# Kernel optimization log

Hardware: AMD Instinct MI355X
Metric: run time of the kernel (lower is better)

## Reference

```python
import jax, jax.numpy as jnp
import numpy as np

T, N, E = 8, 10000, 200000
F_IN, H, OUT = 32, 128, 64
EPS = 1e-5


def setup_inputs() -> dict:
    key = jax.random.key(0)
    ks = jax.random.split(key, 28)
    inp = {}
    inp['x'] = jax.random.normal(ks[0], (T, N, F_IN), jnp.float32)
    inp['edge_index'] = jax.random.randint(ks[1], (2, E), 0, N, dtype=jnp.int32)
    # GCN layer weights (Glorot-ish scale)
    inp['w_gcn0'] = jax.random.normal(ks[2], (F_IN, H), jnp.float32) / np.float32(np.sqrt(F_IN))
    inp['b_gcn0'] = jnp.zeros((H,), jnp.float32)
    inp['w_gcn1'] = jax.random.normal(ks[3], (H, H), jnp.float32) / np.float32(np.sqrt(H))
    inp['b_gcn1'] = jnp.zeros((H,), jnp.float32)
    inp['w_gcn2'] = jax.random.normal(ks[4], (H, H), jnp.float32) / np.float32(np.sqrt(H))
    inp['b_gcn2'] = jnp.zeros((H,), jnp.float32)
    # BatchNorm (eval mode) params for the two inner norms
    for i, kb in zip(range(2), range(5, 9, 2)):
        inp[f'bn_g{i}'] = 1.0 + 0.1 * jax.random.normal(ks[kb], (H,), jnp.float32)
        inp[f'bn_b{i}'] = 0.1 * jax.random.normal(ks[kb + 1], (H,), jnp.float32)
        inp[f'bn_m{i}'] = 0.1 * jax.random.normal(ks[kb + 10], (H,), jnp.float32)
        inp[f'bn_v{i}'] = jax.random.uniform(ks[kb + 11], (H,), jnp.float32, 0.5, 1.5)
    # 3-layer LSTM params, torch gate order (i, f, g, o)
    s = np.float32(1.0 / np.sqrt(OUT))
    dims_in = [H, OUT, OUT]
    for l in range(3):
        k0, k1, k2, k3 = jax.random.split(ks[20 + l], 4)
        inp[f'w_ih_{l}'] = jax.random.uniform(k0, (4 * OUT, dims_in[l]), jnp.float32, -s, s)
        inp[f'w_hh_{l}'] = jax.random.uniform(k1, (4 * OUT, OUT), jnp.float32, -s, s)
        inp[f'b_ih_{l}'] = jax.random.uniform(k2, (4 * OUT,), jnp.float32, -s, s)
        inp[f'b_hh_{l}'] = jax.random.uniform(k3, (4 * OUT,), jnp.float32, -s, s)
    return inp


def reference(x, edge_index, w_gcn0, b_gcn0, w_gcn1, b_gcn1, w_gcn2, b_gcn2,
              bn_g0, bn_b0, bn_m0, bn_v0, bn_g1, bn_b1, bn_m1, bn_v1,
              w_ih_0, w_hh_0, b_ih_0, b_hh_0,
              w_ih_1, w_hh_1, b_ih_1, b_hh_1,
              w_ih_2, w_hh_2, b_ih_2, b_hh_2):
    src, dst = edge_index[0], edge_index[1]
    # symmetric GCN normalization with self-loops: deg = in-degree + 1
    deg = jax.ops.segment_sum(jnp.ones((E,), x.dtype), dst, num_segments=N) + 1.0
    dis = jax.lax.rsqrt(deg)
    coef = dis[src] * dis[dst]          # [E] edge norm
    self_w = dis * dis                   # [N] self-loop norm

    def gcn(h, W, b):
        hw = jnp.einsum('tnf,fo->tno', h, W)                      # [T,N,O]
        msg = hw[:, src, :] * coef[None, :, None]                  # [T,E,O]
        agg = jax.vmap(lambda m: jax.ops.segment_sum(m, dst, num_segments=N))(msg)
        return agg + hw * self_w[None, :, None] + b

    def bn(h, g, b_, m, v):  # eval-mode BatchNorm1d
        return (h - m) * (g * jax.lax.rsqrt(v + EPS)) + b_

    h = bn(jax.nn.relu(gcn(x, w_gcn0, b_gcn0)), bn_g0, bn_b0, bn_m0, bn_v0)
    h = bn(jax.nn.relu(gcn(h, w_gcn1, b_gcn1)), bn_g1, bn_b1, bn_m1, bn_v1)
    h = jax.nn.relu(gcn(h, w_gcn2, b_gcn2))                        # [T,N,H]

    def lstm_layer(xs, Wih, Whh, bih, bhh):
        Hd = Whh.shape[1]
        bias = bih + bhh
        def step(carry, xt):
            hp, cp = carry
            g = xt @ Wih.T + hp @ Whh.T + bias
            i, f, gg, o = jnp.split(g, 4, axis=-1)
            c = jax.nn.sigmoid(f) * cp + jax.nn.sigmoid(i) * jnp.tanh(gg)
            hn = jax.nn.sigmoid(o) * jnp.tanh(c)
            return (hn, c), hn
        z = jnp.zeros((xs.shape[1], Hd), xs.dtype)
        _, ys = jax.lax.scan(step, (z, z), xs)
        return ys  # [T,N,Hd]

    ys = lstm_layer(h, w_ih_0, w_hh_0, b_ih_0, b_hh_0)
    ys = lstm_layer(ys, w_ih_1, w_hh_1, b_ih_1, b_hh_1)
    ys = lstm_layer(ys, w_ih_2, w_hh_2, b_ih_2, b_hh_2)
    return ys[-1]  # [N, OUT] == x[:, -1, :] in the torch code
```

## Files before the change

kernel.cpp:

```cpp
#include <hip/hip_runtime.h>
#include <hip/hip_bf16.h>
#include <math.h>

#define NTHREADS 256
#define T_STEPS 8
#define F_INC 32
#define H_DIM 128
#define O_DIM 64

typedef unsigned short u16;
typedef __attribute__((ext_vector_type(8))) short short8_t;
typedef __attribute__((ext_vector_type(4))) float float4_t;

__device__ __forceinline__ float bf2f(u16 u) {
    return __uint_as_float(((unsigned)u) << 16);
}
__device__ __forceinline__ u16 f2bf(float f) {
    __hip_bfloat16 h = __float2bfloat16(f);
    union { __hip_bfloat16 h; u16 s; } cv; cv.h = h; return cv.s;
}
__device__ __forceinline__ float4 ld_bf4(const u16* p) {
    uint2 u = *(const uint2*)p;
    return make_float4(__uint_as_float(u.x << 16), __uint_as_float(u.x & 0xffff0000u),
                       __uint_as_float(u.y << 16), __uint_as_float(u.y & 0xffff0000u));
}
__device__ __forceinline__ void st_bf4(u16* p, float4 v) {
    ushort4 s = make_ushort4(f2bf(v.x), f2bf(v.y), f2bf(v.z), f2bf(v.w));
    *(ushort4*)p = s;
}
__device__ __forceinline__ float fsig(float x) {
    float xc = fminf(fmaxf(x, -30.f), 30.f);
    float e = __builtin_amdgcn_exp2f(xc * -1.4426950408889634f);
    return __builtin_amdgcn_rcpf(1.0f + e);
}
__device__ __forceinline__ float ftanh(float x) {
    float xc = fminf(fmaxf(x, -15.f), 15.f);
    float e = __builtin_amdgcn_exp2f(xc * -2.8853900817779268f);
    float r = __builtin_amdgcn_rcpf(1.0f + e);
    return fmaf(-2.0f * e, r, 1.0f);
}

__global__ void init_cnt_kernel(int* __restrict__ cnt, int n) {
    int i = blockIdx.x * NTHREADS + threadIdx.x;
    if (i < n) cnt[i] = 0;
}

__global__ void count_kernel(const int* __restrict__ ei, int* __restrict__ cnt, int E) {
    int e = blockIdx.x * NTHREADS + threadIdx.x;
    if (e < E) atomicAdd(&cnt[ei[E + e]], 1);
}

__global__ void scan_part1(const int* __restrict__ cnt, int* __restrict__ bsum, int n) {
    __shared__ int sd[NTHREADS];
    const int i = blockIdx.x * NTHREADS + threadIdx.x;
    sd[threadIdx.x] = (i < n) ? cnt[i] : 0;
    __syncthreads();
    for (int off = 128; off > 0; off >>= 1) {
        if (threadIdx.x < off) sd[threadIdx.x] += sd[threadIdx.x + off];
        __syncthreads();
    }
    if (threadIdx.x == 0) bsum[blockIdx.x] = sd[0];
}
__global__ void scan_part2(const int* __restrict__ bsum, int* __restrict__ boff, int nb) {
    if (threadIdx.x == 0) {
        int s = 0;
        for (int b = 0; b < nb; ++b) { boff[b] = s; s += bsum[b]; }
    }
}
__global__ void scan_part3(const int* __restrict__ cnt, const int* __restrict__ boff,
                           int* __restrict__ rowptr, int* __restrict__ wp,
                           float* __restrict__ dis, float* __restrict__ selfw, int n) {
    __shared__ int sd[NTHREADS];
    const int i = blockIdx.x * NTHREADS + threadIdx.x;
    const int v = (i < n) ? cnt[i] : 0;
    sd[threadIdx.x] = v;
    __syncthreads();
    for (int off = 1; off < NTHREADS; off <<= 1) {
        const int tv = (threadIdx.x >= off) ? sd[threadIdx.x - off] : 0;
        __syncthreads();
        sd[threadIdx.x] += tv;
        __syncthreads();
    }
    const int excl = boff[blockIdx.x] + sd[threadIdx.x] - v;
    if (i < n) {
        rowptr[i] = excl; wp[i] = excl;
        if (i == n - 1) rowptr[n] = excl + v;
        const float d = 1.0f + (float)v;
        dis[i] = rsqrtf(d);
        selfw[i] = 1.0f / d;
    }
}

__global__ void fill_kernel(const int* __restrict__ ei, const float* __restrict__ dis,
                            int* __restrict__ wp, int* __restrict__ csr_src,
                            float* __restrict__ coefA, int E) {
    int e = blockIdx.x * NTHREADS + threadIdx.x;
    if (e < E) {
        int s = ei[e], d = ei[E + e];
        int p = atomicAdd(&wp[d], 1);
        csr_src[p] = s;
        coefA[p] = dis[s] * dis[d];
    }
}

__global__ void wprep_all_kernel(const float* g0, const float* g1, const float* g2,
                                 const float* i0, const float* i1, const float* i2,
                                 const float* h0, const float* h1, const float* h2,
                                 u16* o_g0, u16* o_g1, u16* o_g2,
                                 u16* o_i0, u16* o_i1, u16* o_i2,
                                 u16* o_h0, u16* o_h1, u16* o_h2) {
    const int i = blockIdx.x * NTHREADS + threadIdx.x;
    if (i < 4096)        { o_g0[i] = f2bf(g0[(i & 31) * 128 + (i >> 5)]); }
    else if (i < 20480)  { int j = i - 4096;   o_g1[j] = f2bf(g1[(j & 127) * 128 + (j >> 7)]); }
    else if (i < 36864)  { int j = i - 20480;  o_g2[j] = f2bf(g2[(j & 127) * 128 + (j >> 7)]); }
    else if (i < 69632)  { int j = i - 36864;  o_i0[j] = f2bf(i0[j]); }
    else if (i < 86016)  { int j = i - 69632;  o_i1[j] = f2bf(i1[j]); }
    else if (i < 102400) { int j = i - 86016;  o_i2[j] = f2bf(i2[j]); }
    else if (i < 118784) { int j = i - 102400; o_h0[j] = f2bf(h0[j]); }
    else if (i < 135168) { int j = i - 118784; o_h1[j] = f2bf(h1[j]); }
    else if (i < 151552) { int j = i - 135168; o_h2[j] = f2bf(h2[j]); }
}

__global__ __launch_bounds__(NTHREADS)
void agg32t_kernel(const float* __restrict__ x, const int* __restrict__ rowptr,
                   const int* __restrict__ csrc, const float* __restrict__ coefA,
                   const float* __restrict__ selfw, u16* __restrict__ out, int N) {
    const int t = blockIdx.x;
    const int slot = threadIdx.x >> 3, lane = threadIdx.x & 7;
    const int n = blockIdx.y * 32 + slot;
    if (n >= N) return;
    const int c4 = lane * 4;
    const float* xb = x + (long)t * N * 32;
    const int e0 = rowptr[n], e1 = rowptr[n + 1];
    const float sw = selfw[n];
    const float4 sv = *(const float4*)(xb + (long)n * 32 + c4);
    float4 acc = make_float4(sw * sv.x, sw * sv.y, sw * sv.z, sw * sv.w);
    for (int e = e0; e < e1; ++e) {
        const float wgt = coefA[e];
        const int s = csrc[e];
        const float4 v = *(const float4*)(xb + (long)s * 32 + c4);
        acc.x = fmaf(wgt, v.x, acc.x);
        acc.y = fmaf(wgt, v.y, acc.y);
        acc.z = fmaf(wgt, v.z, acc.z);
        acc.w = fmaf(wgt, v.w, acc.w);
    }
    st_bf4(out + ((long)t * N + n) * 32 + c4, acc);
}

__global__ __launch_bounds__(NTHREADS)
void agg128t_kernel(const u16* __restrict__ h, const int* __restrict__ rowptr,
                    const int* __restrict__ csrc, const float* __restrict__ coefA,
                    const float* __restrict__ selfw, u16* __restrict__ out, int N) {
    const int t = blockIdx.x;
    const int slot = threadIdx.x >> 5, lane = threadIdx.x & 31;
    const int n = blockIdx.y * 8 + slot;
    const int c4 = lane * 4;
    const u16* hb = h + (long)t * N * 128;
    const int e0 = rowptr[n], e1 = rowptr[n + 1];
    const float sw = selfw[n];
    const float4 sv = ld_bf4(hb + (long)n * 128 + c4);
    float4 acc = make_float4(sw * sv.x, sw * sv.y, sw * sv.z, sw * sv.w);
    for (int e = e0; e < e1; ++e) {
        const float wgt = coefA[e];
        const int s = csrc[e];
        const float4 v = ld_bf4(hb + (long)s * 128 + c4);
        acc.x = fmaf(wgt, v.x, acc.x);
        acc.y = fmaf(wgt, v.y, acc.y);
        acc.z = fmaf(wgt, v.z, acc.z);
        acc.w = fmaf(wgt, v.w, acc.w);
    }
    st_bf4(out + ((long)t * N + n) * 128 + c4, acc);
}

template<int K, int EPI, bool OUTBF>
__global__ __launch_bounds__(NTHREADS)
void mfma_gemm_kernel(const u16* __restrict__ A, const u16* __restrict__ Bt,
                      const float* __restrict__ bias0,
                      const float* __restrict__ bng, const float* __restrict__ bnb,
                      const float* __restrict__ bnm, const float* __restrict__ bnv,
                      void* __restrict__ Cout, int ldc) {
    constexpr int KC = (K < 64) ? K : 64;
    constexpr int KP = KC + 8;
    constexpr int KV = KC / 8;
    __shared__ __align__(16) u16 As[128 * KP];
    __shared__ __align__(16) u16 Bs[128 * KP];
    const int tid = threadIdx.x;
    const long row0 = (long)blockIdx.x * 128;
    const int col0 = blockIdx.y * 128;
    const int wid = tid >> 6, lane = tid & 63;
    const int quad = lane >> 4, l16 = lane & 15;

    float4_t acc[2][8];
    #pragma unroll
    for (int rt = 0; rt < 2; ++rt)
        #pragma unroll
        for (int ct = 0; ct < 8; ++ct)
            acc[rt][ct] = (float4_t){0.f, 0.f, 0.f, 0.f};

    const int arow = wid * 32 + l16;
    const int koff = quad * 8;
    for (int ch = 0; ch < K / KC; ++ch) {
        const int kbase = ch * KC;
        for (int p = tid; p < 128 * KV; p += NTHREADS) {
            const int r = p / KV, kv = p % KV;
            *(uint4*)(&As[r * KP + kv * 8]) =
                *(const uint4*)(A + (row0 + r) * K + kbase + kv * 8);
        }
        for (int p = tid; p < 128 * KV; p += NTHREADS) {
            const int r = p / KV, kv = p % KV;
            *(uint4*)(&Bs[r * KP + kv * 8]) =
                *(const uint4*)(Bt + (long)(col0 + r) * K + kbase + kv * 8);
        }
        __syncthreads();
        #pragma unroll
        for (int kc = 0; kc < KC / 32; ++kc) {
            const short8_t a0 = *(const short8_t*)(&As[arow * KP + kc * 32 + koff]);
            const short8_t a1 = *(const short8_t*)(&As[(arow + 16) * KP + kc * 32 + koff]);
            #pragma unroll
            for (int ct = 0; ct < 8; ++ct) {
                const short8_t b = *(const short8_t*)(&Bs[(ct * 16 + l16) * KP + kc * 32 + koff]);
                acc[0][ct] = __builtin_amdgcn_mfma_f32_16x16x32_bf16(a0, b, acc[0][ct], 0, 0, 0);
                acc[1][ct] = __builtin_amdgcn_mfma_f32_16x16x32_bf16(a1, b, acc[1][ct], 0, 0, 0);
            }
        }
        __syncthreads();
    }

    float e_add0[8], e_mul[8], e_add1[8];
    #pragma unroll
    for (int ct = 0; ct < 8; ++ct) {
        const int c = col0 + ct * 16 + l16;
        e_add0[ct] = bias0[c];
        if constexpr (EPI == 2) {
            const float s = bng[c] * rsqrtf(bnv[c] + 1e-5f);
            e_mul[ct] = s;
            e_add1[ct] = bnb[c] - bnm[c] * s;
        }
    }
    #pragma unroll
    for (int rt = 0; rt < 2; ++rt) {
        #pragma unroll
        for (int r = 0; r < 4; ++r) {
            const long row = row0 + wid * 32 + rt * 16 + quad * 4 + r;
            #pragma unroll
            for (int ct = 0; ct < 8; ++ct) {
                float v = fmaxf(acc[rt][ct][r] + e_add0[ct], 0.f);
                if constexpr (EPI == 2) v = fmaf(v, e_mul[ct], e_add1[ct]);
                const long idx = row * (long)ldc + col0 + ct * 16 + l16;
                if constexpr (OUTBF) ((u16*)Cout)[idx] = f2bf(v);
                else ((float*)Cout)[idx] = v;
            }
        }
    }
}

template<int KIN, bool IN_SPLIT, bool LAST>
__global__ __launch_bounds__(NTHREADS, 2)
void lstm_layer_kernel(const u16* __restrict__ in_hi, const u16* __restrict__ in_lo,
                       const u16* __restrict__ wih, const u16* __restrict__ whh,
                       const float* __restrict__ bi, const float* __restrict__ bh,
                       u16* __restrict__ out_hi, u16* __restrict__ out_lo,
                       float* __restrict__ out_f, int N) {
    constexpr int NKS = KIN / 32;
    constexpr int HSTR = 76;
    const int tid = threadIdx.x;
    const int w = tid >> 6, lane = tid & 63;
    const int quad = lane >> 4, l16 = lane & 15;
    const int n0 = blockIdx.x * 16;
    const int u = w * 16 + l16;

    __shared__ __align__(16) u16 hT[2][16][HSTR];
    for (int p = tid; p < 2 * 16 * HSTR; p += NTHREADS) (&hT[0][0][0])[p] = 0;

    short8_t fI[4][NKS], fH[4][2];
    #pragma unroll
    for (int g = 0; g < 4; ++g) {
        #pragma unroll
        for (int ks = 0; ks < NKS; ++ks)
            fI[g][ks] = *(const short8_t*)(wih + (long)(g * 64 + u) * KIN + ks * 32 + quad * 8);
        #pragma unroll
        for (int ks = 0; ks < 2; ++ks)
            fH[g][ks] = *(const short8_t*)(whh + (long)(g * 64 + u) * 64 + ks * 32 + quad * 8);
    }
    float bias[4];
    #pragma unroll
    for (int g = 0; g < 4; ++g) bias[g] = bi[g * 64 + u] + bh[g * 64 + u];
    float cst[4] = {};
    __syncthreads();

    #pragma unroll 1
    for (int t = 0; t < T_STEPS; ++t) {
        short8_t ain[NKS], ainl[NKS];
        const long ibase = ((long)t * N + n0 + l16) * KIN + quad * 8;
        #pragma unroll
        for (int ks = 0; ks < NKS; ++ks) {
            ain[ks] = *(const short8_t*)(in_hi + ibase + ks * 32);
            if constexpr (IN_SPLIT) ainl[ks] = *(const short8_t*)(in_lo + ibase + ks * 32);
        }
        short8_t ah[2], al[2];
        #pragma unroll
        for (int ks = 0; ks < 2; ++ks) {
            ah[ks] = *(const short8_t*)(&hT[0][l16][ks * 32 + quad * 8]);
            al[ks] = *(const short8_t*)(&hT[1][l16][ks * 32 + quad * 8]);
        }
        __syncthreads();

        float4_t acc[4];
        #pragma unroll
        for (int g = 0; g < 4; ++g) acc[g] = (float4_t){bias[g], bias[g], bias[g], bias[g]};
        #pragma unroll
        for (int ks = 0; ks < NKS; ++ks)
            #pragma unroll
            for (int g = 0; g < 4; ++g) {
                acc[g] = __builtin_amdgcn_mfma_f32_16x16x32_bf16(ain[ks], fI[g][ks], acc[g], 0, 0, 0);
                if constexpr (IN_SPLIT)
                    acc[g] = __builtin_amdgcn_mfma_f32_16x16x32_bf16(ainl[ks], fI[g][ks], acc[g], 0, 0, 0);
            }
        #pragma unroll
        for (int ks = 0; ks < 2; ++ks)
            #pragma unroll
            for (int g = 0; g < 4; ++g) {
                acc[g] = __builtin_amdgcn_mfma_f32_16x16x32_bf16(ah[ks], fH[g][ks], acc[g], 0, 0, 0);
                acc[g] = __builtin_amdgcn_mfma_f32_16x16x32_bf16(al[ks], fH[g][ks], acc[g], 0, 0, 0);
            }

        #pragma unroll
        for (int r = 0; r < 4; ++r) {
            const float si = fsig(acc[0][r]);
            const float sf = fsig(acc[1][r]);
            const float gg = ftanh(acc[2][r]);
            const float so = fsig(acc[3][r]);
            const float c = sf * cst[r] + si * gg;
            cst[r] = c;
            const float h = so * ftanh(c);
            const int node = quad * 4 + r;
            const u16 hi = f2bf(h);
            const u16 lo = f2bf(h - bf2f(hi));
            hT[0][node][u] = hi;
            hT[1][node][u] = lo;
            if constexpr (LAST) {
                if (t == T_STEPS - 1) out_f[(long)(n0 + node) * 64 + u] = h;
            } else {
                const long o = ((long)t * N + n0 + node) * 64 + u;
                out_hi[o] = hi;
                out_lo[o] = lo;
            }
        }
        __syncthreads();
    }
}

extern "C" void kernel_launch(void* const* d_in, const int* in_sizes, int n_in,
                              void* d_out, int out_size, void* d_ws, size_t ws_size,
                              hipStream_t stream) {
    (void)n_in; (void)out_size; (void)ws_size;
    const float* x      = (const float*)d_in[0];
    const int*   ei     = (const int*)d_in[1];
    const float* w_gcn0 = (const float*)d_in[2];
    const float* b_gcn0 = (const float*)d_in[3];
    const float* w_gcn1 = (const float*)d_in[4];
    const float* b_gcn1 = (const float*)d_in[5];
    const float* w_gcn2 = (const float*)d_in[6];
    const float* b_gcn2 = (const float*)d_in[7];
    const float* bn_g0  = (const float*)d_in[8];
    const float* bn_b0  = (const float*)d_in[9];
    const float* bn_m0  = (const float*)d_in[10];
    const float* bn_v0  = (const float*)d_in[11];
    const float* bn_g1  = (const float*)d_in[12];
    const float* bn_b1  = (const float*)d_in[13];
    const float* bn_m1  = (const float*)d_in[14];
    const float* bn_v1  = (const float*)d_in[15];
    const float* w_ih_0 = (const float*)d_in[16];
    const float* w_hh_0 = (const float*)d_in[17];
    const float* b_ih_0 = (const float*)d_in[18];
    const float* b_hh_0 = (const float*)d_in[19];
    const float* w_ih_1 = (const float*)d_in[20];
    const float* w_hh_1 = (const float*)d_in[21];
    const float* b_ih_1 = (const float*)d_in[22];
    const float* b_hh_1 = (const float*)d_in[23];
    const float* w_ih_2 = (const float*)d_in[24];
    const float* w_hh_2 = (const float*)d_in[25];
    const float* b_ih_2 = (const float*)d_in[26];
    const float* b_hh_2 = (const float*)d_in[27];

    const int E = in_sizes[1] / 2;
    const int N = in_sizes[0] / (T_STEPS * F_INC);
    const long M = (long)N * T_STEPS;

    char* ws = (char*)d_ws;
    size_t off = 0;
    auto carve = [&](size_t bytes) -> void* {
        void* p = ws + off;
        off += (bytes + 255) & ~(size_t)255;
        return p;
    };
    float* dis     = (float*)carve((size_t)N * 4);
    float* selfw   = (float*)carve((size_t)N * 4);
    float* coefA   = (float*)carve((size_t)E * 4);
    int*   cnt     = (int*)carve((size_t)N * 4);
    int*   rowptr  = (int*)carve((size_t)(N + 1) * 4);
    int*   wp      = (int*)carve((size_t)N * 4);
    int*   csr_src = (int*)carve((size_t)E * 4);
    int*   bsum    = (int*)carve(64 * 4);
    int*   boff    = (int*)carve(64 * 4);
    u16*   hbuf    = (u16*)carve((size_t)M * H_DIM * 2);
    u16*   abuf    = (u16*)carve((size_t)M * H_DIM * 2);
    u16*   pA_hi   = (u16*)carve((size_t)M * O_DIM * 2);
    u16*   pA_lo   = (u16*)carve((size_t)M * O_DIM * 2);
    u16*   pB_hi   = (u16*)carve((size_t)M * O_DIM * 2);
    u16*   pB_lo   = (u16*)carve((size_t)M * O_DIM * 2);
    u16*   wt0     = (u16*)carve((size_t)128 * 32 * 2);
    u16*   wt1     = (u16*)carve((size_t)128 * 128 * 2);
    u16*   wt2     = (u16*)carve((size_t)128 * 128 * 2);
    u16*   wtih0   = (u16*)carve((size_t)256 * 128 * 2);
    u16*   wtih1   = (u16*)carve((size_t)256 * 64 * 2);
    u16*   wtih2   = (u16*)carve((size_t)256 * 64 * 2);
    u16*   whh0b   = (u16*)carve((size_t)256 * 64 * 2);
    u16*   whh1b   = (u16*)carve((size_t)256 * 64 * 2);
    u16*   whh2b   = (u16*)carve((size_t)256 * 64 * 2);

    const dim3 b256(NTHREADS);
    const int gN = (N + NTHREADS - 1) / NTHREADS;
    const int gE = (E + NTHREADS - 1) / NTHREADS;

    init_cnt_kernel<<<gN, b256, 0, stream>>>(cnt, N);
    count_kernel<<<gE, b256, 0, stream>>>(ei, cnt, E);
    scan_part1<<<gN, b256, 0, stream>>>(cnt, bsum, N);
    scan_part2<<<1, 64, 0, stream>>>(bsum, boff, gN);
    scan_part3<<<gN, b256, 0, stream>>>(cnt, boff, rowptr, wp, dis, selfw, N);
    fill_kernel<<<gE, b256, 0, stream>>>(ei, dis, wp, csr_src, coefA, E);

    wprep_all_kernel<<<(151552 + 255) / 256, b256, 0, stream>>>(
        w_gcn0, w_gcn1, w_gcn2, w_ih_0, w_ih_1, w_ih_2, w_hh_0, w_hh_1, w_hh_2,
        wt0, wt1, wt2, wtih0, wtih1, wtih2, whh0b, whh1b, whh2b);

    const int gBlk = (int)(M / 128);
    agg32t_kernel<<<dim3(T_STEPS, (N + 31) / 32), b256, 0, stream>>>(
        x, rowptr, csr_src, coefA, selfw, abuf, N);
    mfma_gemm_kernel<32, 2, true><<<dim3(gBlk, 1), b256, 0, stream>>>(
        abuf, wt0, b_gcn0, bn_g0, bn_b0, bn_m0, bn_v0, hbuf, 128);
    agg128t_kernel<<<dim3(T_STEPS, N / 8), b256, 0, stream>>>(
        hbuf, rowptr, csr_src, coefA, selfw, abuf, N);
    mfma_gemm_kernel<128, 2, true><<<dim3(gBlk, 1), b256, 0, stream>>>(
        abuf, wt1, b_gcn1, bn_g1, bn_b1, bn_m1, bn_v1, hbuf, 128);
    agg128t_kernel<<<dim3(T_STEPS, N / 8), b256, 0, stream>>>(
        hbuf, rowptr, csr_src, coefA, selfw, abuf, N);
    mfma_gemm_kernel<128, 1, true><<<dim3(gBlk, 1), b256, 0, stream>>>(
        abuf, wt2, b_gcn2, nullptr, nullptr, nullptr, nullptr, hbuf, 128);

    const int gL = N / 16;
    lstm_layer_kernel<128, false, false><<<gL, b256, 0, stream>>>(
        hbuf, nullptr, wtih0, whh0b, b_ih_0, b_hh_0, pA_hi, pA_lo, nullptr, N);
    lstm_layer_kernel<64, true, false><<<gL, b256, 0, stream>>>(
        pA_hi, pA_lo, wtih1, whh1b, b_ih_1, b_hh_1, pB_hi, pB_lo, nullptr, N);
    lstm_layer_kernel<64, true, true><<<gL, b256, 0, stream>>>(
        pB_hi, pB_lo, wtih2, whh2b, b_ih_2, b_hh_2, nullptr, nullptr, (float*)d_out, N);
}
```

Before: 426.5 us.

## Split neighbor edges across lanes in GCN aggregation with shuffle reduction

Both aggregation kernels now assign one wavefront per node and spread that node's incoming edges over several lane groups (8 groups for the 32-wide features, 4 for the 128-wide), then combine the partial sums with xor shuffles. The 128-wide kernel also switches to 16-byte loads of 8 bf16 values per lane. The aim is more gathers in flight per node, since each node averages about 20 edges, which shortens the serial per-edge dependency chain and raises memory-level parallelism. The cost is shuffle reduction overhead and idle lanes for low-degree nodes. The grid size assumes N is divisible by 4.

Result: faster. 377.6 us (-11.5%).

```diff
diff --git a/kernel.cpp b/kernel.cpp
--- a/kernel.cpp
+++ b/kernel.cpp
@@ -27,6 +27,12 @@
 __device__ __forceinline__ void st_bf4(u16* p, float4 v) {
     ushort4 s = make_ushort4(f2bf(v.x), f2bf(v.y), f2bf(v.z), f2bf(v.w));
     *(ushort4*)p = s;
+}
+__device__ __forceinline__ void bf8_unpack(uint4 u, float* f) {
+    f[0] = __uint_as_float(u.x << 16); f[1] = __uint_as_float(u.x & 0xffff0000u);
+    f[2] = __uint_as_float(u.y << 16); f[3] = __uint_as_float(u.y & 0xffff0000u);
+    f[4] = __uint_as_float(u.z << 16); f[5] = __uint_as_float(u.z & 0xffff0000u);
+    f[6] = __uint_as_float(u.w << 16); f[7] = __uint_as_float(u.w & 0xffff0000u);
 }
 __device__ __forceinline__ float fsig(float x) {
     float xc = fminf(fmaxf(x, -30.f), 30.f);
@@ -126,25 +132,36 @@
                    const int* __restrict__ csrc, const float* __restrict__ coefA,
                    const float* __restrict__ selfw, u16* __restrict__ out, int N) {
     const int t = blockIdx.x;
-    const int slot = threadIdx.x >> 3, lane = threadIdx.x & 7;
-    const int n = blockIdx.y * 32 + slot;
-    if (n >= N) return;
-    const int c4 = lane * 4;
+    const int n = blockIdx.y * 4 + (threadIdx.x >> 6);
+    const int lane = threadIdx.x & 63;
+    const int split = lane >> 3;
+    const int c4 = (lane & 7) * 4;
     const float* xb = x + (long)t * N * 32;
     const int e0 = rowptr[n], e1 = rowptr[n + 1];
-    const float sw = selfw[n];
-    const float4 sv = *(const float4*)(xb + (long)n * 32 + c4);
-    float4 acc = make_float4(sw * sv.x, sw * sv.y, sw * sv.z, sw * sv.w);
-    for (int e = e0; e < e1; ++e) {
+    float a[4] = {};
+    #pragma unroll 2
+    for (int e = e0 + split; e < e1; e += 8) {
         const float wgt = coefA[e];
         const int s = csrc[e];
         const float4 v = *(const float4*)(xb + (long)s * 32 + c4);
-        acc.x = fmaf(wgt, v.x, acc.x);
-        acc.y = fmaf(wgt, v.y, acc.y);
-        acc.z = fmaf(wgt, v.z, acc.z);
-        acc.w = fmaf(wgt, v.w, acc.w);
-    }
-    st_bf4(out + ((long)t * N + n) * 32 + c4, acc);
+        a[0] = fmaf(wgt, v.x, a[0]);
+        a[1] = fmaf(wgt, v.y, a[1]);
+        a[2] = fmaf(wgt, v.z, a[2]);
+        a[3] = fmaf(wgt, v.w, a[3]);
+    }
+    #pragma unroll
+    for (int j = 0; j < 4; ++j) {
+        a[j] += __shfl_xor(a[j], 8);
+        a[j] += __shfl_xor(a[j], 16);
+        a[j] += __shfl_xor(a[j], 32);
+    }
+    if (split == 0) {
+        const float sw = selfw[n];
+        const float4 sv = *(const float4*)(xb + (long)n * 32 + c4);
+        float4 r = make_float4(fmaf(sw, sv.x, a[0]), fmaf(sw, sv.y, a[1]),
+                               fmaf(sw, sv.z, a[2]), fmaf(sw, sv.w, a[3]));
+        st_bf4(out + ((long)t * N + n) * 32 + c4, r);
+    }
 }
 
 __global__ __launch_bounds__(NTHREADS)
@@ -152,24 +169,42 @@
                     const int* __restrict__ csrc, const float* __restrict__ coefA,
                     const float* __restrict__ selfw, u16* __restrict__ out, int N) {
     const int t = blockIdx.x;
-    const int slot = threadIdx.x >> 5, lane = threadIdx.x & 31;
-    const int n = blockIdx.y * 8 + slot;
-    const int c4 = lane * 4;
+    const int n = blockIdx.y * 4 + (threadIdx.x >> 6);
+    const int lane = threadIdx.x & 63;
+    const int split = lane >> 4;
+    const int c8 = (lane & 15) * 8;
     const u16* hb = h + (long)t * N * 128;
     const int e0 = rowptr[n], e1 = rowptr[n + 1];
-    const float sw = selfw[n];
-    const float4 sv = ld_bf4(hb + (long)n * 128 + c4);
-    float4 acc = make_float4(sw * sv.x, sw * sv.y, sw * sv.z, sw * sv.w);
-    for (int e = e0; e < e1; ++e) {
+    float a[8] = {};
+    #pragma unroll 2
+    for (int e = e0 + split; e < e1; e += 4) {
         const float wgt = coefA[e];
         const int s = csrc[e];
-        const float4 v = ld_bf4(hb + (long)s * 128 + c4);
-        acc.x = fmaf(wgt, v.x, acc.x);
-        acc.y = fmaf(wgt, v.y, acc.y);
-        acc.z = fmaf(wgt, v.z, acc.z);
-        acc.w = fmaf(wgt, v.w, acc.w);
-    }
-    st_bf4(out + ((long)t * N + n) * 128 + c4, acc);
+        const uint4 v = *(const uint4*)(hb + (long)s * 128 + c8);
+        float f[8];
+        bf8_unpack(v, f);
+        #pragma unroll
+        for (int j = 0; j < 8; ++j) a[j] = fmaf(wgt, f[j], a[j]);
+    }
+    #pragma unroll
+    for (int j = 0; j < 8; ++j) {
+        a[j] += __shfl_xor(a[j], 16);
+        a[j] += __shfl_xor(a[j], 32);
+    }
+    if (split == 0) {
+        const float sw = selfw[n];
+        const uint4 sv = *(const uint4*)(hb + (long)n * 128 + c8);
+        float f[8];
+        bf8_unpack(sv, f);
+        ushort4 o0, o1;
+        o0.x = f2bf(fmaf(sw, f[0], a[0])); o0.y = f2bf(fmaf(sw, f[1], a[1]));
+        o0.z = f2bf(fmaf(sw, f[2], a[2])); o0.w = f2bf(fmaf(sw, f[3], a[3]));
+        o1.x = f2bf(fmaf(sw, f[4], a[4])); o1.y = f2bf(fmaf(sw, f[5], a[5]));
+        o1.z = f2bf(fmaf(sw, f[6], a[6])); o1.w = f2bf(fmaf(sw, f[7], a[7]));
+        u16* op = out + ((long)t * N + n) * 128 + c8;
+        *(ushort4*)op = o0;
+        *(ushort4*)(op + 4) = o1;
+    }
 }
 
 template<int K, int EPI, bool OUTBF>
@@ -435,15 +470,15 @@
         wt0, wt1, wt2, wtih0, wtih1, wtih2, whh0b, whh1b, whh2b);
 
     const int gBlk = (int)(M / 128);
-    agg32t_kernel<<<dim3(T_STEPS, (N + 31) / 32), b256, 0, stream>>>(
+    agg32t_kernel<<<dim3(T_STEPS, N / 4), b256, 0, stream>>>(
         x, rowptr, csr_src, coefA, selfw, abuf, N);
     mfma_gemm_kernel<32, 2, true><<<dim3(gBlk, 1), b256, 0, stream>>>(
         abuf, wt0, b_gcn0, bn_g0, bn_b0, bn_m0, bn_v0, hbuf, 128);
-    agg128t_kernel<<<dim3(T_STEPS, N / 8), b256, 0, stream>>>(
+    agg128t_kernel<<<dim3(T_STEPS, N / 4), b256, 0, stream>>>(
         hbuf, rowptr, csr_src, coefA, selfw, abuf, N);
     mfma_gemm_kernel<128, 2, true><<<dim3(gBlk, 1), b256, 0, stream>>>(
         abuf, wt1, b_gcn1, bn_g1, bn_b1, bn_m1, bn_v1, hbuf, 128);
-    agg128t_kernel<<<dim3(T_STEPS, N / 8), b256, 0, stream>>>(
+    agg128t_kernel<<<dim3(T_STEPS, N / 4), b256, 0, stream>>>(
         hbuf, rowptr, csr_src, coefA, selfw, abuf, N);
     mfma_gemm_kernel<128, 1, true><<<dim3(gBlk, 1), b256, 0, stream>>>(
         abuf, wt2, b_gcn2, nullptr, nullptr, nullptr, nullptr, hbuf, 128);
```
